# Kernel optimization log

Measured on AMD Instinct MI355X. Metric: run time of the kernel, lower is better.

## Reference

```python
import jax, jax.numpy as jnp
import numpy as np

N_NODES = 8192
N_EDGES = 262144
D_IN, D_HID, D_OUT = 128, 64, 32
DROP_P = 0.1


def _glorot(key, shape):
    lim = (6.0 / (shape[0] + shape[1])) ** 0.5
    return jax.random.uniform(key, shape, jnp.float32, -lim, lim)


def setup_inputs() -> dict:
    key = jax.random.key(0)
    ks = jax.random.split(key, 8)
    x = jax.random.normal(ks[0], (N_NODES, D_IN), jnp.float32)
    edge_index = jax.random.randint(ks[1], (2, N_EDGES), 0, N_NODES, jnp.int64)
    # GCNConv params: linear weight [in, out] (x @ W) + bias, 3 layers
    W0 = _glorot(ks[2], (D_IN, D_HID)); b0 = jnp.zeros((D_HID,), jnp.float32)
    W1 = _glorot(ks[3], (D_HID, D_HID)); b1 = jnp.zeros((D_HID,), jnp.float32)
    W2 = _glorot(ks[4], (D_HID, D_OUT)); b2 = jnp.zeros((D_OUT,), jnp.float32)
    return {"x": x, "W0": W0, "b0": b0, "W1": W1, "b1": b1,
            "W2": W2, "b2": b2, "edge_index": edge_index}


def _gcn(adj, x, W, b):
    # PyG GCNConv: add self-loops, symmetric normalization D^-1/2 (A+I) D^-1/2
    n = adj.shape[0]
    a = adj + jnp.eye(n, dtype=adj.dtype)
    dinv = jax.lax.rsqrt(a.sum(axis=1))  # deg >= 1 due to self-loop
    a = dinv[:, None] * a * dinv[None, :]
    return a @ (x @ W) + b


def reference(x, W0, b0, W1, b1, W2, b2, edge_index):
    n = x.shape[0]
    # binary dense adjacency of the ORIGINAL graph (to_dense_adj analogue)
    adj0 = jnp.zeros((n, n), x.dtype).at[edge_index[0], edge_index[1]].set(1.0)
    rng = jax.random.key(42)
    params = [(W0, b0), (W1, b1), (W2, b2)]
    adj = adj0
    z = x
    for i, (W, b) in enumerate(params):
        z = jax.nn.relu(_gcn(adj, z, W, b))
        kd, kb = jax.random.split(jax.random.fold_in(rng, i))
        keep = jax.random.bernoulli(kd, 1.0 - DROP_P, z.shape)
        z = jnp.where(keep, z / (1.0 - DROP_P), 0.0)  # Dropout(0.1), train mode
        if i < len(params) - 1:  # last resample never affects the output
            prob = jax.nn.sigmoid(z @ z.T)                      # [N, N]
            sample = (jax.random.uniform(kb, prob.shape) < prob).astype(z.dtype)
            adj = adj0 * sample  # Bernoulli-masked original edges
    return z
```

## Files before the change

kernel.cpp:

```cpp
#include <hip/hip_runtime.h>
#include <stdint.h>
#include <math.h>

#define NN 8192
#define NE 262144
#define WPR 256

struct TFKey { uint32_t a, b; };

__host__ __device__ static inline void tf2x32(uint32_t k0, uint32_t k1,
                                              uint32_t x0, uint32_t x1,
                                              uint32_t* o0, uint32_t* o1) {
  uint32_t ks2 = k0 ^ k1 ^ 0x1BD11BDAu;
#define TF_ROT(x, r) (((x) << (r)) | ((x) >> (32 - (r))))
#define TF_R(r) { x0 += x1; x1 = TF_ROT(x1, r); x1 ^= x0; }
  x0 += k0; x1 += k1;
  TF_R(13) TF_R(15) TF_R(26) TF_R(6)
  x0 += k1;  x1 += ks2 + 1u;
  TF_R(17) TF_R(29) TF_R(16) TF_R(24)
  x0 += ks2; x1 += k0 + 2u;
  TF_R(13) TF_R(15) TF_R(26) TF_R(6)
  x0 += k0;  x1 += k1 + 3u;
  TF_R(17) TF_R(29) TF_R(16) TF_R(24)
  x0 += k1;  x1 += ks2 + 4u;
  TF_R(13) TF_R(15) TF_R(26) TF_R(6)
  x0 += ks2; x1 += k0 + 5u;
  *o0 = x0; *o1 = x1;
#undef TF_R
#undef TF_ROT
}

__device__ static inline float tf_uniform(TFKey k, uint32_t n) {
  uint32_t o0, o1;
  tf2x32(k.a, k.b, 0u, n, &o0, &o1);
  uint32_t bits = o0 ^ o1;
  return __uint_as_float((bits >> 9) | 0x3f800000u) - 1.0f;
}

__global__ __launch_bounds__(256) void k_build(const int* __restrict__ e,
                                               uint32_t* __restrict__ dense,
                                               uint32_t* __restrict__ deg) {
  int ed = blockIdx.x * 256 + threadIdx.x;
  const unsigned long long* p64 = (const unsigned long long*)e;
  unsigned long long v = p64[ed];
  bool int32mode = (__ballot(v >= 8192ull) != 0ull);
  int r, c;
  if (int32mode) { r = e[ed]; c = e[ed + NE]; }
  else { const long long* p = (const long long*)e; r = (int)p[ed]; c = (int)p[ed + NE]; }
  uint32_t bit = 1u << (c & 31);
  uint32_t old = atomicOr(&dense[(size_t)r * WPR + (c >> 5)], bit);
  if (!(old & bit)) atomicAdd(&deg[r], 1u);
}

__global__ __launch_bounds__(256) void k_scan(const uint32_t* __restrict__ deg,
                                              uint32_t* __restrict__ rowptr) {
  __shared__ uint32_t part[256];
  int t = threadIdx.x;
  uint32_t loc[32];
  uint32_t s = 0;
  for (int k = 0; k < 32; ++k) { loc[k] = s; s += deg[t * 32 + k]; }
  part[t] = s;
  __syncthreads();
  for (int off = 1; off < 256; off <<= 1) {
    uint32_t v = (t >= off) ? part[t - off] : 0u;
    __syncthreads();
    part[t] += v;
    __syncthreads();
  }
  uint32_t base = (t == 0) ? 0u : part[t - 1];
  for (int k = 0; k < 32; ++k) rowptr[t * 32 + k] = base + loc[k];
  if (t == 255) rowptr[8192] = part[255];
}

__global__ __launch_bounds__(256) void k_fill(const uint32_t* __restrict__ dense,
                                              const uint32_t* __restrict__ rowptr,
                                              uint16_t* __restrict__ cols,
                                              uint16_t* __restrict__ rows) {
  int lane = threadIdx.x & 63;
  int i = blockIdx.x * 4 + (threadIdx.x >> 6);
  const uint4* row = (const uint4*)(dense + (size_t)i * WPR);
  uint4 v = row[lane];
  uint32_t w[4] = { v.x, v.y, v.z, v.w };
  int cnt = __popc(w[0]) + __popc(w[1]) + __popc(w[2]) + __popc(w[3]);
  int pre = cnt;
  for (int s = 1; s < 64; s <<= 1) {
    int o = __shfl_up(pre, s, 64);
    if (lane >= s) pre += o;
  }
  pre -= cnt;
  uint32_t pos = rowptr[i] + (uint32_t)pre;
  for (int wi = 0; wi < 4; ++wi) {
    uint32_t word = w[wi];
    while (word) {
      int b = __ffs(word) - 1;
      word &= word - 1;
      cols[pos] = (uint16_t)(lane * 128 + wi * 32 + b);
      rows[pos] = (uint16_t)i;
      ++pos;
    }
  }
}

template<int K, int N>
__global__ __launch_bounds__(256) void k_dg(const float* __restrict__ A,
                                            const float* __restrict__ Wb,
                                            float* __restrict__ H,
                                            const uint32_t* __restrict__ rowptr,
                                            const uint8_t* __restrict__ mask,
                                            float* __restrict__ dinv) {
  constexpr int GB = NN * N / 256;
  if (blockIdx.x < GB) {
    int t = blockIdx.x * 256 + threadIdx.x;
    int i = t / N, c = t % N;
    double a0 = 0.0, a1 = 0.0;
#pragma unroll 8
    for (int k = 0; k < K; k += 2) {
      a0 += (double)A[(size_t)i * K + k] * (double)Wb[(size_t)k * N + c];
      a1 += (double)A[(size_t)i * K + k + 1] * (double)Wb[(size_t)(k + 1) * N + c];
    }
    H[t] = (float)(a0 + a1);
  } else {
    int lane = threadIdx.x & 63;
    int i = (blockIdx.x - GB) * 4 + (threadIdx.x >> 6);
    uint32_t s0 = rowptr[i], s1 = rowptr[i + 1];
    int c = 0;
    for (uint32_t e = s0 + lane; e < s1; e += 64) c += mask ? (int)mask[e] : 1;
    for (int s = 32; s; s >>= 1) c += __shfl_xor(c, s, 64);
    if (lane == 0) dinv[i] = (float)(1.0 / sqrt((double)(c + 1)));
  }
}

template<int D>
__global__ __launch_bounds__(256) void k_agg(const uint32_t* __restrict__ rowptr,
                                             const uint16_t* __restrict__ cols,
                                             const uint8_t* __restrict__ mask,
                                             const float* __restrict__ h,
                                             const float* __restrict__ dinv,
                                             const float* __restrict__ bias,
                                             TFKey kd, float* __restrict__ zout) {
  int lane = threadIdx.x & 63;
  int i = blockIdx.x * 4 + (threadIdx.x >> 6);
  bool act = lane < D;
  float di = dinv[i];
  uint32_t s0 = rowptr[i], s1 = rowptr[i + 1];
  double a0 = 0.0, a1 = 0.0;
  uint32_t e = s0;
  for (; e + 1 < s1; e += 2) {
    int j0 = cols[e], j1 = cols[e + 1];
    bool m0 = !mask || mask[e], m1 = !mask || mask[e + 1];
    if (act) {
      if (m0) { float c0 = di * dinv[j0]; a0 += (double)c0 * (double)h[(size_t)j0 * D + lane]; }
      if (m1) { float c1 = di * dinv[j1]; a1 += (double)c1 * (double)h[(size_t)j1 * D + lane]; }
    }
  }
  if (e < s1 && (!mask || mask[e]) && act) {
    int j = cols[e];
    float c = di * dinv[j];
    a0 += (double)c * (double)h[(size_t)j * D + lane];
  }
  if (act) {
    double acc = a0 + a1;
    float cI = di * di;
    acc += (double)cI * (double)h[(size_t)i * D + lane];
    float s = (float)acc;
    float pre = fmaxf(s + bias[lane], 0.0f);
    float u = tf_uniform(kd, (uint32_t)(i * D + lane));
    zout[(size_t)i * D + lane] = (u < 0.9f) ? (pre / 0.9f) : 0.0f;
  }
}

__global__ __launch_bounds__(256) void k_sample_e(const uint32_t* __restrict__ rowptr,
                                                  const uint16_t* __restrict__ rows,
                                                  const uint16_t* __restrict__ cols,
                                                  const float* __restrict__ z,
                                                  TFKey kb,
                                                  uint8_t* __restrict__ mask) {
  uint32_t e = blockIdx.x * 256 + threadIdx.x;
  uint32_t nnz = rowptr[8192];
  if (e >= nnz) return;
  uint32_t i = rows[e], j = cols[e];
  const float4* zi = (const float4*)(z + (size_t)i * 64);
  const float4* zj = (const float4*)(z + (size_t)j * 64);
  double p0 = 0.0, p1 = 0.0, p2 = 0.0, p3 = 0.0;
#pragma unroll
  for (int q = 0; q < 16; q += 2) {
    float4 a = zi[q], b = zj[q];
    float4 c = zi[q + 1], d = zj[q + 1];
    p0 += (double)a.x * (double)b.x + (double)a.y * (double)b.y;
    p1 += (double)a.z * (double)b.z + (double)a.w * (double)b.w;
    p2 += (double)c.x * (double)d.x + (double)c.y * (double)d.y;
    p3 += (double)c.z * (double)d.z + (double)c.w * (double)d.w;
  }
  double p = (p0 + p1) + (p2 + p3);
  float dot32 = (float)p;
  float prob = (float)(1.0 / (1.0 + exp(-(double)dot32)));
  uint32_t n = (i << 13) | j;
  float u = tf_uniform(kb, n);
  mask[e] = (u < prob) ? 1u : 0u;
}

extern "C" void kernel_launch(void* const* d_in, const int* in_sizes, int n_in,
                              void* d_out, int out_size, void* d_ws, size_t ws_size,
                              hipStream_t stream) {
  (void)in_sizes; (void)n_in; (void)out_size; (void)ws_size;
  const float* x  = (const float*)d_in[0];
  const float* W0 = (const float*)d_in[1];
  const float* b0 = (const float*)d_in[2];
  const float* W1 = (const float*)d_in[3];
  const float* b1 = (const float*)d_in[4];
  const float* W2 = (const float*)d_in[5];
  const float* b2 = (const float*)d_in[6];
  const int* ei = (const int*)d_in[7];
  float* out = (float*)d_out;

  uint8_t* base = (uint8_t*)d_ws;
  uint32_t* dense = (uint32_t*)(base);
  float* h        = (float*)(base);
  float* z        = (float*)(base + 2097152);
  uint32_t* deg   = (uint32_t*)(base + 8388608);
  uint32_t* rowptr= (uint32_t*)(base + 8388608 + 65536);
  uint16_t* cols  = (uint16_t*)(base + 8388608 + 131072);
  uint16_t* rows  = (uint16_t*)(base + 8388608 + 655360);
  uint8_t*  mask  = (uint8_t*)(base + 8388608 + 1179648);
  float*    dinv  = (float*)(base + 8388608 + 1441792);

  TFKey kd[3], kb[3];
  for (uint32_t i = 0; i < 3; ++i) {
    uint32_t la, lb;
    tf2x32(0u, 42u, 0u, i, &la, &lb);
    tf2x32(la, lb, 0u, 0u, &kd[i].a, &kd[i].b);
    tf2x32(la, lb, 0u, 1u, &kb[i].a, &kb[i].b);
  }

  (void)hipMemsetAsync(dense, 0, (size_t)NN * WPR * 4 + 32768, stream);
  k_build<<<NE / 256, 256, 0, stream>>>(ei, dense, deg);
  k_scan <<<1, 256, 0, stream>>>(deg, rowptr);
  k_fill <<<NN / 4, 256, 0, stream>>>(dense, rowptr, cols, rows);

  k_dg<128, 64><<<NN * 64 / 256 + NN / 4, 256, 0, stream>>>(x, W0, h, rowptr, nullptr, dinv);
  k_agg<64><<<NN / 4, 256, 0, stream>>>(rowptr, cols, nullptr, h, dinv, b0, kd[0], z);
  k_sample_e<<<NE / 256, 256, 0, stream>>>(rowptr, rows, cols, z, kb[0], mask);

  k_dg<64, 64><<<NN * 64 / 256 + NN / 4, 256, 0, stream>>>(z, W1, h, rowptr, mask, dinv);
  k_agg<64><<<NN / 4, 256, 0, stream>>>(rowptr, cols, mask, h, dinv, b1, kd[1], z);
  k_sample_e<<<NE / 256, 256, 0, stream>>>(rowptr, rows, cols, z, kb[1], mask);

  k_dg<64, 32><<<NN * 32 / 256 + NN / 4, 256, 0, stream>>>(z, W2, h, rowptr, mask, dinv);
  k_agg<32><<<NN / 4, 256, 0, stream>>>(rowptr, cols, mask, h, dinv, b2, kd[2], out);
}
```

Baseline: 234.5 us.

## Pack edge row/col into one word and count sampled degrees with atomics

Edge row and column indices are packed into a single 32-bit word, replacing two uint16 arrays. The sampling kernel now atomically counts kept edges per row, so the degree pass in k_dg becomes a per-node rsqrt instead of a warp reduction over the mask. The scan kernel also loads degrees with vector loads. This trades extra atomics in the sampling kernel for removing a per-row mask reduction, and adds two count buffers to the workspace memset.

```diff
diff --git a/kernel.cpp b/kernel.cpp
--- a/kernel.cpp
+++ b/kernel.cpp
@@ -56,9 +56,17 @@
                                               uint32_t* __restrict__ rowptr) {
   __shared__ uint32_t part[256];
   int t = threadIdx.x;
+  uint32_t d[32];
+  const uint4* dv = (const uint4*)(deg + t * 32);
+#pragma unroll
+  for (int q = 0; q < 8; ++q) {
+    uint4 v = dv[q];
+    d[q * 4] = v.x; d[q * 4 + 1] = v.y; d[q * 4 + 2] = v.z; d[q * 4 + 3] = v.w;
+  }
   uint32_t loc[32];
   uint32_t s = 0;
-  for (int k = 0; k < 32; ++k) { loc[k] = s; s += deg[t * 32 + k]; }
+#pragma unroll
+  for (int k = 0; k < 32; ++k) { loc[k] = s; s += d[k]; }
   part[t] = s;
   __syncthreads();
   for (int off = 1; off < 256; off <<= 1) {
@@ -68,14 +76,14 @@
     __syncthreads();
   }
   uint32_t base = (t == 0) ? 0u : part[t - 1];
+#pragma unroll
   for (int k = 0; k < 32; ++k) rowptr[t * 32 + k] = base + loc[k];
   if (t == 255) rowptr[8192] = part[255];
 }
 
 __global__ __launch_bounds__(256) void k_fill(const uint32_t* __restrict__ dense,
                                               const uint32_t* __restrict__ rowptr,
-                                              uint16_t* __restrict__ cols,
-                                              uint16_t* __restrict__ rows) {
+                                              uint32_t* __restrict__ pack) {
   int lane = threadIdx.x & 63;
   int i = blockIdx.x * 4 + (threadIdx.x >> 6);
   const uint4* row = (const uint4*)(dense + (size_t)i * WPR);
@@ -89,14 +97,13 @@
   }
   pre -= cnt;
   uint32_t pos = rowptr[i] + (uint32_t)pre;
+  uint32_t ibase = ((uint32_t)i << 13);
   for (int wi = 0; wi < 4; ++wi) {
     uint32_t word = w[wi];
     while (word) {
       int b = __ffs(word) - 1;
       word &= word - 1;
-      cols[pos] = (uint16_t)(lane * 128 + wi * 32 + b);
-      rows[pos] = (uint16_t)i;
-      ++pos;
+      pack[pos++] = ibase | (uint32_t)(lane * 128 + wi * 32 + b);
     }
   }
 }
@@ -105,8 +112,7 @@
 __global__ __launch_bounds__(256) void k_dg(const float* __restrict__ A,
                                             const float* __restrict__ Wb,
                                             float* __restrict__ H,
-                                            const uint32_t* __restrict__ rowptr,
-                                            const uint8_t* __restrict__ mask,
+                                            const uint32_t* __restrict__ cnt,
                                             float* __restrict__ dinv) {
   constexpr int GB = NN * N / 256;
   if (blockIdx.x < GB) {
@@ -120,19 +126,14 @@
     }
     H[t] = (float)(a0 + a1);
   } else {
-    int lane = threadIdx.x & 63;
-    int i = (blockIdx.x - GB) * 4 + (threadIdx.x >> 6);
-    uint32_t s0 = rowptr[i], s1 = rowptr[i + 1];
-    int c = 0;
-    for (uint32_t e = s0 + lane; e < s1; e += 64) c += mask ? (int)mask[e] : 1;
-    for (int s = 32; s; s >>= 1) c += __shfl_xor(c, s, 64);
-    if (lane == 0) dinv[i] = (float)(1.0 / sqrt((double)(c + 1)));
+    int i = (blockIdx.x - GB) * 256 + threadIdx.x;
+    if (i < NN) dinv[i] = (float)(1.0 / sqrt((double)(cnt[i] + 1)));
   }
 }
 
 template<int D>
 __global__ __launch_bounds__(256) void k_agg(const uint32_t* __restrict__ rowptr,
-                                             const uint16_t* __restrict__ cols,
+                                             const uint32_t* __restrict__ pack,
                                              const uint8_t* __restrict__ mask,
                                              const float* __restrict__ h,
                                              const float* __restrict__ dinv,
@@ -146,7 +147,7 @@
   double a0 = 0.0, a1 = 0.0;
   uint32_t e = s0;
   for (; e + 1 < s1; e += 2) {
-    int j0 = cols[e], j1 = cols[e + 1];
+    int j0 = pack[e] & 8191, j1 = pack[e + 1] & 8191;
     bool m0 = !mask || mask[e], m1 = !mask || mask[e + 1];
     if (act) {
       if (m0) { float c0 = di * dinv[j0]; a0 += (double)c0 * (double)h[(size_t)j0 * D + lane]; }
@@ -154,7 +155,7 @@
     }
   }
   if (e < s1 && (!mask || mask[e]) && act) {
-    int j = cols[e];
+    int j = pack[e] & 8191;
     float c = di * dinv[j];
     a0 += (double)c * (double)h[(size_t)j * D + lane];
   }
@@ -170,15 +171,16 @@
 }
 
 __global__ __launch_bounds__(256) void k_sample_e(const uint32_t* __restrict__ rowptr,
-                                                  const uint16_t* __restrict__ rows,
-                                                  const uint16_t* __restrict__ cols,
+                                                  const uint32_t* __restrict__ pack,
                                                   const float* __restrict__ z,
                                                   TFKey kb,
-                                                  uint8_t* __restrict__ mask) {
+                                                  uint8_t* __restrict__ mask,
+                                                  uint32_t* __restrict__ cnt) {
   uint32_t e = blockIdx.x * 256 + threadIdx.x;
   uint32_t nnz = rowptr[8192];
   if (e >= nnz) return;
-  uint32_t i = rows[e], j = cols[e];
+  uint32_t n = pack[e];
+  uint32_t i = n >> 13, j = n & 8191;
   const float4* zi = (const float4*)(z + (size_t)i * 64);
   const float4* zj = (const float4*)(z + (size_t)j * 64);
   double p0 = 0.0, p1 = 0.0, p2 = 0.0, p3 = 0.0;
@@ -194,9 +196,10 @@
   double p = (p0 + p1) + (p2 + p3);
   float dot32 = (float)p;
   float prob = (float)(1.0 / (1.0 + exp(-(double)dot32)));
-  uint32_t n = (i << 13) | j;
   float u = tf_uniform(kb, n);
-  mask[e] = (u < prob) ? 1u : 0u;
+  uint8_t mb = (u < prob) ? 1u : 0u;
+  mask[e] = mb;
+  if (mb) atomicAdd(&cnt[i], 1u);
 }
 
 extern "C" void kernel_launch(void* const* d_in, const int* in_sizes, int n_in,
@@ -218,11 +221,12 @@
   float* h        = (float*)(base);
   float* z        = (float*)(base + 2097152);
   uint32_t* deg   = (uint32_t*)(base + 8388608);
-  uint32_t* rowptr= (uint32_t*)(base + 8388608 + 65536);
-  uint16_t* cols  = (uint16_t*)(base + 8388608 + 131072);
-  uint16_t* rows  = (uint16_t*)(base + 8388608 + 655360);
-  uint8_t*  mask  = (uint8_t*)(base + 8388608 + 1179648);
-  float*    dinv  = (float*)(base + 8388608 + 1441792);
+  uint32_t* cnt0  = (uint32_t*)(base + 8388608 + 32768);
+  uint32_t* cnt1  = (uint32_t*)(base + 8388608 + 65536);
+  uint32_t* rowptr= (uint32_t*)(base + 8388608 + 98304);
+  uint32_t* pack  = (uint32_t*)(base + 8388608 + 163840);
+  uint8_t*  mask  = (uint8_t*)(base + 8388608 + 1212416);
+  float*    dinv  = (float*)(base + 8388608 + 1474560);
 
   TFKey kd[3], kb[3];
   for (uint32_t i = 0; i < 3; ++i) {
@@ -232,19 +236,19 @@
     tf2x32(la, lb, 0u, 1u, &kb[i].a, &kb[i].b);
   }
 
-  (void)hipMemsetAsync(dense, 0, (size_t)NN * WPR * 4 + 32768, stream);
+  (void)hipMemsetAsync(dense, 0, (size_t)NN * WPR * 4 + 98304, stream);
   k_build<<<NE / 256, 256, 0, stream>>>(ei, dense, deg);
   k_scan <<<1, 256, 0, stream>>>(deg, rowptr);
-  k_fill <<<NN / 4, 256, 0, stream>>>(dense, rowptr, cols, rows);
-
-  k_dg<128, 64><<<NN * 64 / 256 + NN / 4, 256, 0, stream>>>(x, W0, h, rowptr, nullptr, dinv);
-  k_agg<64><<<NN / 4, 256, 0, stream>>>(rowptr, cols, nullptr, h, dinv, b0, kd[0], z);
-  k_sample_e<<<NE / 256, 256, 0, stream>>>(rowptr, rows, cols, z, kb[0], mask);
-
-  k_dg<64, 64><<<NN * 64 / 256 + NN / 4, 256, 0, stream>>>(z, W1, h, rowptr, mask, dinv);
-  k_agg<64><<<NN / 4, 256, 0, stream>>>(rowptr, cols, mask, h, dinv, b1, kd[1], z);
-  k_sample_e<<<NE / 256, 256, 0, stream>>>(rowptr, rows, cols, z, kb[1], mask);
-
-  k_dg<64, 32><<<NN * 32 / 256 + NN / 4, 256, 0, stream>>>(z, W2, h, rowptr, mask, dinv);
-  k_agg<32><<<NN / 4, 256, 0, stream>>>(rowptr, cols, mask, h, dinv, b2, kd[2], out);
-}
+  k_fill <<<NN / 4, 256, 0, stream>>>(dense, rowptr, pack);
+
+  k_dg<128, 64><<<NN * 64 / 256 + NN / 256, 256, 0, stream>>>(x, W0, h, deg, dinv);
+  k_agg<64><<<NN / 4, 256, 0, stream>>>(rowptr, pack, nullptr, h, dinv, b0, kd[0], z);
+  k_sample_e<<<NE / 256, 256, 0, stream>>>(rowptr, pack, z, kb[0], mask, cnt0);
+
+  k_dg<64, 64><<<NN * 64 / 256 + NN / 256, 256, 0, stream>>>(z, W1, h, cnt0, dinv);
+  k_agg<64><<<NN / 4, 256, 0, stream>>>(rowptr, pack, mask, h, dinv, b1, kd[1], z);
+  k_sample_e<<<NE / 256, 256, 0, stream>>>(rowptr, pack, z, kb[1], mask, cnt1);
+
+  k_dg<64, 32><<<NN * 32 / 256 + NN / 256, 256, 0, stream>>>(z, W2, h, cnt1, dinv);
+  k_agg<32><<<NN / 4, 256, 0, stream>>>(rowptr, pack, mask, h, dinv, b2, kd[2], out);
+}
```

Measured after the change: 255.6 us. 1.09x slower.
